# Kernel optimization log

Hardware: AMD Instinct MI355X
Metric: run time of the kernel (lower is better)

The kernel has to match this reference:

```python
import jax, jax.numpy as jnp
import numpy as np

N_NODES = 10000
N_EDGES = 320000
H = 256
L = 3
EPS = 1e-5


def _mlp2(x, w1, b1, w2, b2):
    # Linear -> ReLU -> Linear
    return jax.nn.relu(x @ w1 + b1) @ w2 + b2


def _layer_norm(x, g, b):
    mu = jnp.mean(x, axis=-1, keepdims=True)
    var = jnp.var(x, axis=-1, keepdims=True)
    return (x - mu) * jax.lax.rsqrt(var + EPS) * g + b


def setup_inputs() -> dict:
    key = jax.random.key(0)
    ks = jax.random.split(key, 24)
    s = 0.02
    inp = {
        "node_features": jax.random.normal(ks[0], (N_NODES, H), dtype=jnp.float32),
        "edge_index": jax.random.randint(ks[1], (2, N_EDGES), 0, N_NODES, dtype=jnp.int64),
        # node encoder (Linear 256->256, ReLU, Linear 256->256)
        "ne_w1": jax.random.normal(ks[2], (H, H), dtype=jnp.float32) * s,
        "ne_b1": jnp.zeros((H,), jnp.float32),
        "ne_w2": jax.random.normal(ks[3], (H, H), dtype=jnp.float32) * s,
        "ne_b2": jnp.zeros((H,), jnp.float32),
        # per-layer message MLP (2H->H, ReLU, H->H), stacked over L layers
        "msg_w1": jax.random.normal(ks[4], (L, 2 * H, H), dtype=jnp.float32) * s,
        "msg_b1": jnp.zeros((L, H), jnp.float32),
        "msg_w2": jax.random.normal(ks[5], (L, H, H), dtype=jnp.float32) * s,
        "msg_b2": jnp.zeros((L, H), jnp.float32),
        # per-layer update MLP (2H->H, ReLU, H->H)
        "upd_w1": jax.random.normal(ks[6], (L, 2 * H, H), dtype=jnp.float32) * s,
        "upd_b1": jnp.zeros((L, H), jnp.float32),
        "upd_w2": jax.random.normal(ks[7], (L, H, H), dtype=jnp.float32) * s,
        "upd_b2": jnp.zeros((L, H), jnp.float32),
        # per-layer LayerNorm
        "ln_g": jnp.ones((L, H), jnp.float32),
        "ln_b": jnp.zeros((L, H), jnp.float32),
        # readout MLP
        "ro_w1": jax.random.normal(ks[8], (H, H), dtype=jnp.float32) * s,
        "ro_b1": jnp.zeros((H,), jnp.float32),
        "ro_w2": jax.random.normal(ks[9], (H, H), dtype=jnp.float32) * s,
        "ro_b2": jnp.zeros((H,), jnp.float32),
    }
    return inp


def reference(node_features, edge_index, ne_w1, ne_b1, ne_w2, ne_b2,
              msg_w1, msg_b1, msg_w2, msg_b2,
              upd_w1, upd_b1, upd_w2, upd_b2,
              ln_g, ln_b, ro_w1, ro_b1, ro_w2, ro_b2):
    n_nodes = node_features.shape[0]
    src, dst = edge_index[0], edge_index[1]

    # node encoder
    x = _mlp2(node_features, ne_w1, ne_b1, ne_w2, ne_b2)  # [N, H]

    # message passing layers (edge_attr is unused in the original layer)
    for l in range(L):
        cat_e = jnp.concatenate([x[src], x[dst]], axis=-1)          # [E, 2H]
        messages = _mlp2(cat_e, msg_w1[l], msg_b1[l], msg_w2[l], msg_b2[l])  # [E, H]
        aggregated = jax.ops.segment_sum(messages, dst, num_segments=n_nodes)  # [N, H]
        cat_n = jnp.concatenate([x, aggregated], axis=-1)           # [N, 2H]
        updated = _mlp2(cat_n, upd_w1[l], upd_b1[l], upd_w2[l], upd_b2[l])
        x = _layer_norm(x + updated, ln_g[l], ln_b[l])

    # mean readout
    g = jnp.mean(x, axis=0)  # [H]
    return _mlp2(g, ro_w1, ro_b1, ro_w2, ro_b2)  # [H]
```

## Files before the change

kernel.cpp:

```cpp
#include <hip/hip_runtime.h>

#define NN 10000
#define NE 320000
#define HD 256
#define NL 3

typedef unsigned short ushort_t;
typedef __attribute__((ext_vector_type(8))) short bf16x8;
typedef __attribute__((ext_vector_type(4))) float f32x4;

#define MFMA __builtin_amdgcn_mfma_f32_16x16x32_bf16

__device__ __forceinline__ unsigned short f2bf(float x) {
    unsigned u = __float_as_uint(x);
    unsigned rounding = 0x7FFFu + ((u >> 16) & 1u);
    return (unsigned short)((u + rounding) >> 16);
}
__device__ __forceinline__ float bf2f(unsigned short u) {
    return __uint_as_float(((unsigned)u) << 16);
}
__device__ __forceinline__ bf16x8 cvt8(float4 lo, float4 hi) {
    bf16x8 r;
    r[0] = (short)f2bf(lo.x); r[1] = (short)f2bf(lo.y);
    r[2] = (short)f2bf(lo.z); r[3] = (short)f2bf(lo.w);
    r[4] = (short)f2bf(hi.x); r[5] = (short)f2bf(hi.y);
    r[6] = (short)f2bf(hi.z); r[7] = (short)f2bf(hi.w);
    return r;
}
__device__ __forceinline__ void dma16(const void* g, void* l) {
    __builtin_amdgcn_global_load_lds(
        (const __attribute__((address_space(1))) unsigned int*)g,
        (__attribute__((address_space(3))) unsigned int*)l, 16, 0, 0);
}


__global__ void hist_deg(const int* __restrict__ dst, int* __restrict__ deg, int E) {
    int e = blockIdx.x * blockDim.x + threadIdx.x;
    if (e < E) atomicAdd(&deg[dst[e]], 1);
}

__global__ __launch_bounds__(1024) void scan_csr(const int* __restrict__ deg,
                                                 int* __restrict__ row_start,
                                                 int* __restrict__ cursor,
                                                 float* __restrict__ degf,
                                                 float* __restrict__ gsum, int n) {
    __shared__ int wsum[16];
    __shared__ int carry_s;
    int tid = threadIdx.x, lane = tid & 63, wid = tid >> 6;
    if (tid < HD) gsum[tid] = 0.f;
    if (tid == 0) carry_s = 0;
    __syncthreads();
    for (int base = 0; base < n; base += 1024) {
        int i = base + tid;
        int v = (i < n) ? deg[i] : 0;
        int s = v;
        #pragma unroll
        for (int off = 1; off < 64; off <<= 1) {
            int t = __shfl_up(s, off);
            if (lane >= off) s += t;
        }
        if (lane == 63) wsum[wid] = s;
        __syncthreads();
        if (wid == 0 && lane < 16) {
            int ws = wsum[lane];
            #pragma unroll
            for (int off = 1; off < 16; off <<= 1) {
                int t = __shfl_up(ws, off);
                if (lane >= off) ws += t;
            }
            wsum[lane] = ws;
        }
        __syncthreads();
        int carry = carry_s;
        int wpre = (wid > 0) ? wsum[wid - 1] : 0;
        int incl = carry + wpre + s;
        int excl = incl - v;
        if (i < n) { row_start[i] = excl; cursor[i] = excl; degf[i] = (float)v; }
        __syncthreads();
        if (tid == 1023) carry_s = incl;
        __syncthreads();
    }
    if (tid == 0) row_start[n] = carry_s;
}

__global__ void scatter_src(const int* __restrict__ src, const int* __restrict__ dst,
                            int* __restrict__ cursor, int* __restrict__ src_sorted, int E) {
    int e = blockIdx.x * blockDim.x + threadIdx.x;
    if (e < E) {
        int pos = atomicAdd(&cursor[dst[e]], 1);
        src_sorted[pos] = src[e];
    }
}


struct TDesc { const float* src; ushort_t* dst; int transpose; };
struct TArgs { TDesc d[20]; };

__global__ __launch_bounds__(256) void conv_t(TArgs args) {
    __shared__ ushort_t tile[64][65];
    const float* src = args.d[blockIdx.y].src;
    ushort_t* dst = args.d[blockIdx.y].dst;
    int tr = args.d[blockIdx.y].transpose;
    int t = blockIdx.x;
    int r0 = (t >> 2) * 64, c0 = (t & 3) * 64;
    int tid = threadIdx.x;
    int rr = tid >> 4, cc4 = (tid & 15) * 4;
    if (!tr) {
        #pragma unroll
        for (int i = 0; i < 4; ++i) {
            int r = r0 + rr + i * 16;
            float4 v = *(const float4*)(src + (size_t)r * HD + c0 + cc4);
            ushort4 o = { f2bf(v.x), f2bf(v.y), f2bf(v.z), f2bf(v.w) };
            *(ushort4*)(dst + (size_t)r * HD + c0 + cc4) = o;
        }
        return;
    }
    #pragma unroll
    for (int i = 0; i < 4; ++i) {
        int r = rr + i * 16;
        float4 v = *(const float4*)(src + (size_t)(r0 + r) * HD + c0 + cc4);
        tile[cc4 + 0][r] = f2bf(v.x);
        tile[cc4 + 1][r] = f2bf(v.y);
        tile[cc4 + 2][r] = f2bf(v.z);
        tile[cc4 + 3][r] = f2bf(v.w);
    }
    __syncthreads();
    #pragma unroll
    for (int i = 0; i < 4; ++i) {
        int c = rr + i * 16;
        ushort4 o = { tile[c][cc4], tile[c][cc4 + 1], tile[c][cc4 + 2], tile[c][cc4 + 3] };
        *(ushort4*)(dst + (size_t)(c0 + c) * HD + r0 + cc4) = o;
    }
}

__global__ __launch_bounds__(256) void bias_compose(const float* __restrict__ mb2,
                                                    const float* __restrict__ uw1,
                                                    float* __restrict__ out) {
    int l = blockIdx.x, c = threadIdx.x;
    const float* b2l = mb2 + (size_t)l * HD;
    const float* u1b = uw1 + (size_t)l * 2 * HD * HD + (size_t)HD * HD;
    float s = 0.f;
    for (int k = 0; k < HD; ++k) s += b2l[k] * u1b[(size_t)k * HD + c];
    out[(size_t)l * HD + c] = s;
}

__global__ __launch_bounds__(256) void gemm_w2u(
    const ushort_t* __restrict__ Abase, const ushort_t* __restrict__ Btbase,
    ushort_t* __restrict__ outBase)
{
    const ushort_t* A  = Abase  + (size_t)blockIdx.z * HD * HD;
    const ushort_t* Bt = Btbase + (size_t)blockIdx.z * HD * HD;
    ushort_t* outB     = outBase + (size_t)blockIdx.z * HD * HD;
    int tid = threadIdx.x;
    int wid = tid >> 6, lane = tid & 63;
    int wm = wid >> 1, wn = wid & 1;
    int row0 = blockIdx.x * 64 + wm * 32;
    int col0 = blockIdx.y * 64 + wn * 32;
    int lm = lane & 15, lk = (lane >> 4) * 8;
    f32x4 acc[2][2] = {};
    const ushort_t* a0p = A + (size_t)(row0 + lm) * HD + lk;
    const ushort_t* a1p = A + (size_t)(row0 + 16 + lm) * HD + lk;
    const ushort_t* b0p = Bt + (size_t)(col0 + lm) * HD + lk;
    const ushort_t* b1p = Bt + (size_t)(col0 + 16 + lm) * HD + lk;
    #pragma unroll
    for (int k0 = 0; k0 < HD; k0 += 32) {
        bf16x8 a0 = *(const bf16x8*)(a0p + k0);
        bf16x8 a1 = *(const bf16x8*)(a1p + k0);
        bf16x8 b0 = *(const bf16x8*)(b0p + k0);
        bf16x8 b1 = *(const bf16x8*)(b1p + k0);
        acc[0][0] = MFMA(a0, b0, acc[0][0], 0, 0, 0);
        acc[0][1] = MFMA(a0, b1, acc[0][1], 0, 0, 0);
        acc[1][0] = MFMA(a1, b0, acc[1][0], 0, 0, 0);
        acc[1][1] = MFMA(a1, b1, acc[1][1], 0, 0, 0);
    }
    int orow = (lane >> 4) * 4;
    #pragma unroll
    for (int mi = 0; mi < 2; ++mi)
        #pragma unroll
        for (int r = 0; r < 4; ++r) {
            int row = row0 + mi * 16 + orow + r;
            #pragma unroll
            for (int ni = 0; ni < 2; ++ni) {
                int col = col0 + ni * 16 + lm;
                outB[(size_t)row * HD + col] = f2bf(acc[mi][ni][r]);
            }
        }
}

__device__ __forceinline__ int swz(int row, int byte_in_row) {
    return row * 512 + (byte_in_row ^ ((row & 7) << 4));
}


__global__ __launch_bounds__(512, 4) void enc_pq(
    const float* __restrict__ A, const ushort_t* __restrict__ B1t,
    const ushort_t* __restrict__ B2t,
    const float* __restrict__ b1, const float* __restrict__ b2,
    const ushort_t* __restrict__ Pw1t, const ushort_t* __restrict__ Pw1b,
    const float* __restrict__ pqb1,
    float* __restrict__ xF, ushort_t* __restrict__ xB,
    ushort_t* __restrict__ P, float* __restrict__ Q, int M)
{
    __shared__ char wbuf[2][2][16384];
    __shared__ char hid[16 * 512];
    int tid = threadIdx.x;
    int w = tid >> 6, lane = tid & 63;
    int lm = lane & 15, q = lane >> 4;
    int row0 = blockIdx.x * 16;
    int col0 = w * 32;
    int cA = col0 + lm, cB = col0 + 16 + lm;

    auto stageB = [&](const ushort_t* Bt, int k0, char* dst16k, int cc) {
        int col = cc * 16 + (lane >> 2);
        int qs = (lane & 3) ^ (col & 3) ^ ((col >> 2) & 3);
        dma16((const char*)Bt + (size_t)col * 512 + k0 * 2 + qs * 16, dst16k + cc * 1024);
    };
    auto readB = [&](const char* base, int ni) -> bf16x8 {
        int col = col0 + 16 * ni + lm;
        int q2 = q ^ (col & 3) ^ ((col >> 2) & 3);
        return *(const bf16x8*)(base + col * 64 + q2 * 16);
    };

    for (int c = w; c < 16; c += 8) stageB(B1t, 0, wbuf[0][0], c);

    float b1v[2] = { b1[cA], b1[cB] };
    float b2v[2] = { b2[cA], b2[cB] };
    float pqv[2] = { pqb1[cA], pqb1[cB] };
    bf16x8 areg[8];
    {
        const float* ap = A + (size_t)(row0 + lm) * HD + q * 8;
        #pragma unroll
        for (int j = 0; j < 8; ++j) {
            float4 lo = *(const float4*)(ap + j * 32);
            float4 hi = *(const float4*)(ap + j * 32 + 4);
            areg[j] = cvt8(lo, hi);
        }
    }
    __syncthreads();

    f32x4 acc[2] = {};
    #pragma unroll
    for (int j = 0; j < 8; ++j) {
        if (j < 7) {
            int k0 = (j + 1) * 32, p = (j + 1) & 1;
            for (int c = w; c < 16; c += 8) stageB(B1t, k0, wbuf[p][0], c);
        }
        int p = j & 1;
        acc[0] = MFMA(areg[j], readB(wbuf[p][0], 0), acc[0], 0, 0, 0);
        acc[1] = MFMA(areg[j], readB(wbuf[p][0], 1), acc[1], 0, 0, 0);
        __syncthreads();
    }

    for (int c = w; c < 16; c += 8) stageB(B2t, 0, wbuf[0][0], c);
    #pragma unroll
    for (int ni = 0; ni < 2; ++ni) {
        int col = col0 + 16 * ni + lm;
        #pragma unroll
        for (int r = 0; r < 4; ++r) {
            int row = 4 * q + r;
            float v = fmaxf(acc[ni][r] + b1v[ni], 0.f);
            *(ushort_t*)(hid + swz(row, col * 2)) = f2bf(v);
        }
    }
    __syncthreads();

    f32x4 acc2[2] = {};
    #pragma unroll
    for (int j = 0; j < 8; ++j) {
        if (j < 7) {
            int k0 = (j + 1) * 32, p = (j + 1) & 1;
            for (int c = w; c < 16; c += 8) stageB(B2t, k0, wbuf[p][0], c);
        }
        int p = j & 1;
        int bk = (j * 32 + q * 8) * 2;
        bf16x8 a = *(const bf16x8*)(hid + swz(lm, bk));
        acc2[0] = MFMA(a, readB(wbuf[p][0], 0), acc2[0], 0, 0, 0);
        acc2[1] = MFMA(a, readB(wbuf[p][0], 1), acc2[1], 0, 0, 0);
        __syncthreads();
    }

    for (int c = w; c < 32; c += 8) {
        if (c < 16) stageB(Pw1t, 0, wbuf[0][0], c);
        else        stageB(Pw1b, 0, wbuf[0][1], c - 16);
    }
    #pragma unroll
    for (int ni = 0; ni < 2; ++ni) {
        int col = col0 + 16 * ni + lm;
        #pragma unroll
        for (int r = 0; r < 4; ++r) {
            int row = 4 * q + r;
            int grow = row0 + row;
            float v = acc2[ni][r] + b2v[ni];
            *(ushort_t*)(hid + swz(row, col * 2)) = f2bf(v);
            xF[(size_t)grow * HD + col] = v;
            xB[(size_t)grow * HD + col] = f2bf(v);
        }
    }
    __syncthreads();

    f32x4 aP[2] = {}, aQ[2] = {};
    #pragma unroll
    for (int j = 0; j < 8; ++j) {
        if (j < 7) {
            int k0 = (j + 1) * 32, p = (j + 1) & 1;
            for (int c = w; c < 32; c += 8) {
                if (c < 16) stageB(Pw1t, k0, wbuf[p][0], c);
                else        stageB(Pw1b, k0, wbuf[p][1], c - 16);
            }
        }
        int p = j & 1;
        int bk = (j * 32 + q * 8) * 2;
        bf16x8 a = *(const bf16x8*)(hid + swz(lm, bk));
        #pragma unroll
        for (int ni = 0; ni < 2; ++ni) {
            aP[ni] = MFMA(a, readB(wbuf[p][0], ni), aP[ni], 0, 0, 0);
            aQ[ni] = MFMA(a, readB(wbuf[p][1], ni), aQ[ni], 0, 0, 0);
        }
        __syncthreads();
    }
    #pragma unroll
    for (int r = 0; r < 4; ++r) {
        int grow = row0 + 4 * q + r;
        #pragma unroll
        for (int ni = 0; ni < 2; ++ni) {
            int col = col0 + 16 * ni + lm;
            P[(size_t)grow * HD + col] = f2bf(aP[ni][r]);
            Q[(size_t)grow * HD + col] = aQ[ni][r] + pqv[ni];
        }
    }
}


__global__ __launch_bounds__(256) void edge_agg(
    const ushort_t* __restrict__ Pb, const float* __restrict__ Qf,
    const int* __restrict__ row_start, const int* __restrict__ srcs,
    ushort_t* __restrict__ Haggb)
{
    int node = blockIdx.x * 4 + (threadIdx.x >> 6);
    int lane = threadIdx.x & 63;
    int c4 = lane * 4;
    float4 qb = *(const float4*)(Qf + (size_t)node * HD + c4);
    float4 acc = {0.f, 0.f, 0.f, 0.f};
    int j = row_start[node], e = row_start[node + 1];
    for (; j + 8 <= e; j += 8) {
        ushort4 p[8];
        #pragma unroll
        for (int u = 0; u < 8; ++u) {
            int s = srcs[j + u];
            p[u] = *(const ushort4*)(Pb + (size_t)s * HD + c4);
        }
        #pragma unroll
        for (int u = 0; u < 8; ++u) {
            acc.x += fmaxf(bf2f(p[u].x) + qb.x, 0.f);
            acc.y += fmaxf(bf2f(p[u].y) + qb.y, 0.f);
            acc.z += fmaxf(bf2f(p[u].z) + qb.z, 0.f);
            acc.w += fmaxf(bf2f(p[u].w) + qb.w, 0.f);
        }
    }
    for (; j < e; ++j) {
        int s0 = srcs[j];
        ushort4 p0 = *(const ushort4*)(Pb + (size_t)s0 * HD + c4);
        acc.x += fmaxf(bf2f(p0.x) + qb.x, 0.f);
        acc.y += fmaxf(bf2f(p0.y) + qb.y, 0.f);
        acc.z += fmaxf(bf2f(p0.z) + qb.z, 0.f);
        acc.w += fmaxf(bf2f(p0.w) + qb.w, 0.f);
    }
    ushort4 o = { f2bf(acc.x), f2bf(acc.y), f2bf(acc.z), f2bf(acc.w) };
    *(ushort4*)(Haggb + (size_t)node * HD + c4) = o;
}


__global__ __launch_bounds__(512, 4) void upd_ln(
    const ushort_t* __restrict__ xb, const ushort_t* __restrict__ Hb,
    const ushort_t* __restrict__ B1t, const ushort_t* __restrict__ B2t,
    const ushort_t* __restrict__ B3t,
    const float* __restrict__ degf,
    const float* __restrict__ b1, const float* __restrict__ bias2,
    const float* __restrict__ b3,
    const float* __restrict__ g, const float* __restrict__ bb,
    const ushort_t* __restrict__ Pw1t, const ushort_t* __restrict__ Pw1b,
    const float* __restrict__ pqb1,
    float* __restrict__ gsum,
    float* __restrict__ xF, ushort_t* __restrict__ xB,
    ushort_t* __restrict__ P, float* __restrict__ Q, int M)
{
    __shared__ char wbuf[2][2][16384];
    __shared__ char abuf[2][2][1024];
    __shared__ char hid[16 * 512];
    __shared__ float sS[8][16], sQ[8][16], muv[16], ivv[16];

    int tid = threadIdx.x;
    int w = tid >> 6, lane = tid & 63;
    int lm = lane & 15, q = lane >> 4;
    int row0 = blockIdx.x * 16;
    int col0 = w * 32;
    int cA = col0 + lm, cB = col0 + 16 + lm;

    float b1v[2] = { b1[cA], b1[cB] };
    float bzv[2] = { bias2[cA], bias2[cB] };
    float b3v[2] = { b3[cA], b3[cB] };
    float gv[2]  = { g[cA],  g[cB]  };
    float bbv[2] = { bb[cA], bb[cB] };
    float pqv[2] = { Pw1t ? pqb1[cA] : 0.f, Pw1t ? pqb1[cB] : 0.f };
    float dgv[4], res[2][4];
    #pragma unroll
    for (int r = 0; r < 4; ++r) {
        int row = 4 * q + r;
        dgv[r] = degf[row0 + row];
        res[0][r] = xF[(size_t)(row0 + row) * HD + cA];
        res[1][r] = xF[(size_t)(row0 + row) * HD + cB];
    }

    auto stageB = [&](const ushort_t* Bt, int k0, char* dst16k, int cc) {
        int col = cc * 16 + (lane >> 2);
        int qs = (lane & 3) ^ (col & 3) ^ ((col >> 2) & 3);
        dma16((const char*)Bt + (size_t)col * 512 + k0 * 2 + qs * 16, dst16k + cc * 1024);
    };
    auto stageA = [&](const ushort_t* X, int k0, char* dst1k) {
        int row = lane >> 2;
        int qs = (lane & 3) ^ (row & 3) ^ ((row >> 2) & 3);
        dma16((const char*)X + (size_t)(row0 + row) * 512 + k0 * 2 + qs * 16, dst1k);
    };
    auto readB = [&](const char* base, int ni) -> bf16x8 {
        int col = col0 + 16 * ni + lm;
        int q2 = q ^ (col & 3) ^ ((col >> 2) & 3);
        return *(const bf16x8*)(base + col * 64 + q2 * 16);
    };
    auto readA = [&](const char* base) -> bf16x8 {
        int q2 = q ^ (lm & 3) ^ ((lm >> 2) & 3);
        return *(const bf16x8*)(base + lm * 64 + q2 * 16);
    };

    auto stage1 = [&](int j, int p) {
        int k0 = j * 32;
        for (int c = w; c < 34; c += 8) {
            if (c < 16)       stageB(B1t, k0, wbuf[p][0], c);
            else if (c < 32)  stageB(B2t, k0, wbuf[p][1], c - 16);
            else if (c == 32) stageA(xb, k0, abuf[p][0]);
            else              stageA(Hb, k0, abuf[p][1]);
        }
    };
    f32x4 acc[2] = {};
    stage1(0, 0);
    __syncthreads();
    #pragma unroll
    for (int j = 0; j < 8; ++j) {
        if (j < 7) stage1(j + 1, (j + 1) & 1);
        int p = j & 1;
        bf16x8 ax = readA(abuf[p][0]);
        bf16x8 ah = readA(abuf[p][1]);
        #pragma unroll
        for (int ni = 0; ni < 2; ++ni) {
            bf16x8 bu = readB(wbuf[p][0], ni);
            bf16x8 bw = readB(wbuf[p][1], ni);
            acc[ni] = MFMA(ax, bu, acc[ni], 0, 0, 0);
            acc[ni] = MFMA(ah, bw, acc[ni], 0, 0, 0);
        }
        __syncthreads();
    }

    for (int c = w; c < 16; c += 8) stageB(B3t, 0, wbuf[0][0], c);
    #pragma unroll
    for (int r = 0; r < 4; ++r) {
        int row = 4 * q + r;
        #pragma unroll
        for (int ni = 0; ni < 2; ++ni) {
            int col = col0 + 16 * ni + lm;
            float v = fmaxf(acc[ni][r] + b1v[ni] + dgv[r] * bzv[ni], 0.f);
            *(ushort_t*)(hid + swz(row, col * 2)) = f2bf(v);
        }
    }
    __syncthreads();

    f32x4 acc2[2] = {};
    #pragma unroll
    for (int j = 0; j < 8; ++j) {
        if (j < 7) {
            int k0 = (j + 1) * 32, p = (j + 1) & 1;
            for (int c = w; c < 16; c += 8) stageB(B3t, k0, wbuf[p][0], c);
        }
        int p = j & 1;
        int bk = (j * 32 + q * 8) * 2;
        bf16x8 a = *(const bf16x8*)(hid + swz(lm, bk));
        #pragma unroll
        for (int ni = 0; ni < 2; ++ni) {
            bf16x8 b = readB(wbuf[p][0], ni);
            acc2[ni] = MFMA(a, b, acc2[ni], 0, 0, 0);
        }
        __syncthreads();
    }

    if (Pw1t) {
        for (int c = w; c < 32; c += 8) {
            if (c < 16) stageB(Pw1t, 0, wbuf[0][0], c);
            else        stageB(Pw1b, 0, wbuf[0][1], c - 16);
        }
    }
    #pragma unroll
    for (int r = 0; r < 4; ++r) {
        float s = 0.f, qq = 0.f;
        #pragma unroll
        for (int ni = 0; ni < 2; ++ni) {
            float v = acc2[ni][r] + b3v[ni] + res[ni][r];
            acc2[ni][r] = v;
            s += v; qq += v * v;
        }
        #pragma unroll
        for (int off = 1; off < 16; off <<= 1) {
            s += __shfl_xor(s, off);
            qq += __shfl_xor(qq, off);
        }
        if (lm == 0) {
            int row = 4 * q + r;
            sS[w][row] = s; sQ[w][row] = qq;
        }
    }
    __syncthreads();
    if (tid < 16) {
        float s = 0.f, qq = 0.f;
        #pragma unroll
        for (int i = 0; i < 8; ++i) { s += sS[i][tid]; qq += sQ[i][tid]; }
        float mu = s * (1.0f / HD);
        float var = qq * (1.0f / HD) - mu * mu;
        muv[tid] = mu;
        ivv[tid] = rsqrtf(var + 1e-5f);
    }
    __syncthreads();
    float csum[2] = {0.f, 0.f};
    #pragma unroll
    for (int r = 0; r < 4; ++r) {
        int row = 4 * q + r;
        int grow = row0 + row;
        float mu = muv[row], iv = ivv[row];
        #pragma unroll
        for (int ni = 0; ni < 2; ++ni) {
            int col = col0 + 16 * ni + lm;
            float o = (acc2[ni][r] - mu) * iv * gv[ni] + bbv[ni];
            *(ushort_t*)(hid + swz(row, col * 2)) = f2bf(o);
            xF[(size_t)grow * HD + col] = o;
            xB[(size_t)grow * HD + col] = f2bf(o);
            csum[ni] += o;
        }
    }
    if (gsum) {
        #pragma unroll
        for (int ni = 0; ni < 2; ++ni) {
            float s = csum[ni];
            s += __shfl_xor(s, 16);
            s += __shfl_xor(s, 32);
            if (q == 0) atomicAdd(&gsum[col0 + 16 * ni + lm], s);
        }
    }

    if (Pw1t) {
        __syncthreads();
        f32x4 aP[2] = {}, aQ[2] = {};
        #pragma unroll
        for (int j = 0; j < 8; ++j) {
            if (j < 7) {
                int k0 = (j + 1) * 32, p = (j + 1) & 1;
                for (int c = w; c < 32; c += 8) {
                    if (c < 16) stageB(Pw1t, k0, wbuf[p][0], c);
                    else        stageB(Pw1b, k0, wbuf[p][1], c - 16);
                }
            }
            int p = j & 1;
            int bk = (j * 32 + q * 8) * 2;
            bf16x8 a = *(const bf16x8*)(hid + swz(lm, bk));
            #pragma unroll
            for (int ni = 0; ni < 2; ++ni) {
                bf16x8 bp = readB(wbuf[p][0], ni);
                bf16x8 bq = readB(wbuf[p][1], ni);
                aP[ni] = MFMA(a, bp, aP[ni], 0, 0, 0);
                aQ[ni] = MFMA(a, bq, aQ[ni], 0, 0, 0);
            }
            __syncthreads();
        }
        #pragma unroll
        for (int r = 0; r < 4; ++r) {
            int grow = row0 + 4 * q + r;
            #pragma unroll
            for (int ni = 0; ni < 2; ++ni) {
                int col = col0 + 16 * ni + lm;
                P[(size_t)grow * HD + col] = f2bf(aP[ni][r]);
                Q[(size_t)grow * HD + col] = aQ[ni][r] + pqv[ni];
            }
        }
    }
}


__global__ __launch_bounds__(256) void readout_mlp(
    const float* __restrict__ gsum,
    const float* __restrict__ w1, const float* __restrict__ b1,
    const float* __restrict__ w2, const float* __restrict__ b2,
    float* __restrict__ out, float invn)
{
    __shared__ float gl[HD], h1[HD];
    int c = threadIdx.x;
    gl[c] = gsum[c] * invn;
    __syncthreads();
    float a = b1[c];
    for (int k = 0; k < HD; ++k) a += gl[k] * w1[k * HD + c];
    h1[c] = fmaxf(a, 0.f);
    __syncthreads();
    float o = b2[c];
    for (int k = 0; k < HD; ++k) o += h1[k] * w2[k * HD + c];
    out[c] = o;
}


extern "C" void kernel_launch(void* const* d_in, const int* in_sizes, int n_in,
                              void* d_out, int out_size, void* d_ws, size_t ws_size,
                              hipStream_t stream) {
    const float* nf    = (const float*)d_in[0];
    const int*   ei    = (const int*)d_in[1];
    const float* ne_w1 = (const float*)d_in[2];
    const float* ne_b1 = (const float*)d_in[3];
    const float* ne_w2 = (const float*)d_in[4];
    const float* ne_b2 = (const float*)d_in[5];
    const float* mw1   = (const float*)d_in[6];
    const float* mb1   = (const float*)d_in[7];
    const float* mw2   = (const float*)d_in[8];
    const float* mb2   = (const float*)d_in[9];
    const float* uw1   = (const float*)d_in[10];
    const float* ub1   = (const float*)d_in[11];
    const float* uw2   = (const float*)d_in[12];
    const float* ub2   = (const float*)d_in[13];
    const float* lng   = (const float*)d_in[14];
    const float* lnb   = (const float*)d_in[15];
    const float* rw1   = (const float*)d_in[16];
    const float* rb1   = (const float*)d_in[17];
    const float* rw2   = (const float*)d_in[18];
    const float* rb2   = (const float*)d_in[19];

    const int* e_src = ei;
    const int* e_dst = ei + NE;

    char* w = (char*)d_ws;
    size_t off = 0;
    auto alloc = [&](size_t bytes) -> void* {
        void* p = w + off;
        off = (off + bytes + 255) & ~(size_t)255;
        return p;
    };
    const size_t NF32 = (size_t)NN * HD * sizeof(float);
    const size_t NF16 = (size_t)NN * HD * sizeof(ushort_t);
    const size_t WM16 = (size_t)HD * HD * sizeof(ushort_t);

    float* x    = (float*)alloc(NF32);
    float* Qf   = (float*)alloc(NF32);
    float* gsum = (float*)alloc(HD * sizeof(float));
    float* degf = (float*)alloc(NN * sizeof(float));
    float* b2u1 = (float*)alloc(NL * HD * sizeof(float));

    ushort_t* xb    = (ushort_t*)alloc(NF16);
    ushort_t* Pb    = (ushort_t*)alloc(NF16);
    ushort_t* Haggb = (ushort_t*)alloc(NF16);
    ushort_t* neT1  = (ushort_t*)alloc(WM16);
    ushort_t* neT2  = (ushort_t*)alloc(WM16);
    ushort_t* w1tT  = (ushort_t*)alloc(NL * WM16);
    ushort_t* w1bT  = (ushort_t*)alloc(NL * WM16);
    ushort_t* u1tT  = (ushort_t*)alloc(NL * WM16);
    ushort_t* u1bT  = (ushort_t*)alloc(NL * WM16);
    ushort_t* u2T   = (ushort_t*)alloc(NL * WM16);
    ushort_t* w2uT  = (ushort_t*)alloc(NL * WM16);
    ushort_t* w2rmb = (ushort_t*)alloc(NL * WM16);

    int* deg       = (int*)alloc(NN * sizeof(int));
    int* row_start = (int*)alloc((NN + 1) * sizeof(int));
    int* cursor    = (int*)alloc(NN * sizeof(int));
    int* srcs      = (int*)alloc(NE * sizeof(int));

    hipMemsetAsync(deg, 0, NN * sizeof(int), stream);

    hist_deg<<<(NE + 255) / 256, 256, 0, stream>>>(e_dst, deg, NE);
    scan_csr<<<1, 1024, 0, stream>>>(deg, row_start, cursor, degf, gsum, NN);
    scatter_src<<<(NE + 255) / 256, 256, 0, stream>>>(e_src, e_dst, cursor, srcs, NE);

    TArgs ta;
    ta.d[0] = { ne_w1, neT1, 1 };
    ta.d[1] = { ne_w2, neT2, 1 };
    for (int l = 0; l < NL; ++l) {
        const float* w1l = mw1 + (size_t)l * 2 * HD * HD;
        const float* u1l = uw1 + (size_t)l * 2 * HD * HD;
        ta.d[2 + l]  = { w1l,                       w1tT + (size_t)l * HD * HD, 1 };
        ta.d[5 + l]  = { w1l + (size_t)HD * HD,     w1bT + (size_t)l * HD * HD, 1 };
        ta.d[8 + l]  = { u1l,                       u1tT + (size_t)l * HD * HD, 1 };
        ta.d[11 + l] = { u1l + (size_t)HD * HD,     u1bT + (size_t)l * HD * HD, 1 };
        ta.d[14 + l] = { uw2 + (size_t)l * HD * HD, u2T + (size_t)l * HD * HD, 1 };
        ta.d[17 + l] = { mw2 + (size_t)l * HD * HD, w2rmb + (size_t)l * HD * HD, 0 };
    }
    conv_t<<<dim3(16, 20), 256, 0, stream>>>(ta);
    bias_compose<<<NL, 256, 0, stream>>>(mb2, uw1, b2u1);
    gemm_w2u<<<dim3(4, 4, NL), 256, 0, stream>>>(u1bT, w2rmb, w2uT);

    enc_pq<<<NN / 16, 512, 0, stream>>>(nf, neT1, neT2, ne_b1, ne_b2,
                                        w1tT, w1bT, mb1, x, xb, Pb, Qf, NN);

    for (int l = 0; l < NL; ++l) {
        edge_agg<<<NN / 4, 256, 0, stream>>>(Pb, Qf, row_start, srcs, Haggb);
        int nl = l + 1;
        const ushort_t* pw1t = (nl < NL) ? w1tT + (size_t)nl * HD * HD : nullptr;
        const ushort_t* pw1b = (nl < NL) ? w1bT + (size_t)nl * HD * HD : nullptr;
        const float*    pqb1 = (nl < NL) ? mb1 + (size_t)nl * HD : nullptr;
        float* gs = (l == NL - 1) ? gsum : nullptr;
        upd_ln<<<NN / 16, 512, 0, stream>>>(
            xb, Haggb, u1tT + (size_t)l * HD * HD, w2uT + (size_t)l * HD * HD,
            u2T + (size_t)l * HD * HD, degf,
            ub1 + (size_t)l * HD, b2u1 + (size_t)l * HD, ub2 + (size_t)l * HD,
            lng + (size_t)l * HD, lnb + (size_t)l * HD,
            pw1t, pw1b, pqb1, gs, x, xb, Pb, Qf, NN);
    }

    readout_mlp<<<1, 256, 0, stream>>>(gsum, rw1, rb1, rw2, rb2, (float*)d_out, 1.0f / NN);
}
```

Measured before the change: 326.6 us.

## Pipeline weight DMA two stages ahead with explicit vmcnt waits in node kernels

```diff
diff --git a/kernel.cpp b/kernel.cpp
--- a/kernel.cpp
+++ b/kernel.cpp
@@ -10,6 +10,11 @@
 typedef __attribute__((ext_vector_type(4))) float f32x4;
 
 #define MFMA __builtin_amdgcn_mfma_f32_16x16x32_bf16
+
+#define WAITV(N) asm volatile("s_waitcnt vmcnt(" #N ")" ::: "memory")
+#define HARDBAR() do { __builtin_amdgcn_s_barrier(); __builtin_amdgcn_sched_barrier(0); } while (0)
+#define LGKMBAR() do { asm volatile("s_waitcnt lgkmcnt(0)" ::: "memory"); \
+                       __builtin_amdgcn_s_barrier(); __builtin_amdgcn_sched_barrier(0); } while (0)
 
 __device__ __forceinline__ unsigned short f2bf(float x) {
     unsigned u = __float_as_uint(x);
@@ -210,10 +215,25 @@
     int col0 = w * 32;
     int cA = col0 + lm, cB = col0 + 16 + lm;
 
-    auto stageB = [&](const ushort_t* Bt, int k0, char* dst16k, int cc) {
-        int col = cc * 16 + (lane >> 2);
-        int qs = (lane & 3) ^ (col & 3) ^ ((col >> 2) & 3);
-        dma16((const char*)Bt + (size_t)col * 512 + k0 * 2 + qs * 16, dst16k + cc * 1024);
+    auto stage1 = [&](const ushort_t* M0, int k0, int p) {
+        #pragma unroll
+        for (int i = 0; i < 2; ++i) {
+            int cc = 2 * w + i;
+            int col = cc * 16 + (lane >> 2);
+            int qs = (lane & 3) ^ (col & 3) ^ ((col >> 2) & 3);
+            dma16((const char*)M0 + (size_t)col * 512 + k0 * 2 + qs * 16, wbuf[p][0] + cc * 1024);
+        }
+    };
+    auto stage2 = [&](const ushort_t* M0, const ushort_t* M1, int k0, int p) {
+        #pragma unroll
+        for (int i = 0; i < 4; ++i) {
+            int c = 4 * w + i;
+            int m = c >> 4, cc = c & 15;
+            const ushort_t* Mt = m ? M1 : M0;
+            int col = cc * 16 + (lane >> 2);
+            int qs = (lane & 3) ^ (col & 3) ^ ((col >> 2) & 3);
+            dma16((const char*)Mt + (size_t)col * 512 + k0 * 2 + qs * 16, wbuf[p][m] + cc * 1024);
+        }
     };
     auto readB = [&](const char* base, int ni) -> bf16x8 {
         int col = col0 + 16 * ni + lm;
@@ -221,8 +241,8 @@
         return *(const bf16x8*)(base + col * 64 + q2 * 16);
     };
 
-    for (int c = w; c < 16; c += 8) stageB(B1t, 0, wbuf[0][0], c);
-
+    stage1(B1t, 0, 0);
+    stage1(B1t, 32, 1);
     float b1v[2] = { b1[cA], b1[cB] };
     float b2v[2] = { b2[cA], b2[cB] };
     float pqv[2] = { pqb1[cA], pqb1[cB] };
@@ -236,22 +256,21 @@
             areg[j] = cvt8(lo, hi);
         }
     }
-    __syncthreads();
 
     f32x4 acc[2] = {};
     #pragma unroll
     for (int j = 0; j < 8; ++j) {
-        if (j < 7) {
-            int k0 = (j + 1) * 32, p = (j + 1) & 1;
-            for (int c = w; c < 16; c += 8) stageB(B1t, k0, wbuf[p][0], c);
-        }
         int p = j & 1;
+        if (j < 7) { WAITV(2); } else { WAITV(0); }
+        HARDBAR();
         acc[0] = MFMA(areg[j], readB(wbuf[p][0], 0), acc[0], 0, 0, 0);
         acc[1] = MFMA(areg[j], readB(wbuf[p][0], 1), acc[1], 0, 0, 0);
-        __syncthreads();
-    }
-
-    for (int c = w; c < 16; c += 8) stageB(B2t, 0, wbuf[0][0], c);
+        LGKMBAR();
+        if (j < 6) stage1(B1t, (j + 2) * 32, p);
+    }
+
+    stage1(B2t, 0, 0);
+    stage1(B2t, 32, 1);
     #pragma unroll
     for (int ni = 0; ni < 2; ++ni) {
         int col = col0 + 16 * ni + lm;
@@ -262,27 +281,24 @@
             *(ushort_t*)(hid + swz(row, col * 2)) = f2bf(v);
         }
     }
-    __syncthreads();
+    LGKMBAR();
 
     f32x4 acc2[2] = {};
     #pragma unroll
     for (int j = 0; j < 8; ++j) {
-        if (j < 7) {
-            int k0 = (j + 1) * 32, p = (j + 1) & 1;
-            for (int c = w; c < 16; c += 8) stageB(B2t, k0, wbuf[p][0], c);
-        }
         int p = j & 1;
+        if (j < 7) { WAITV(2); } else { WAITV(0); }
+        HARDBAR();
         int bk = (j * 32 + q * 8) * 2;
         bf16x8 a = *(const bf16x8*)(hid + swz(lm, bk));
         acc2[0] = MFMA(a, readB(wbuf[p][0], 0), acc2[0], 0, 0, 0);
         acc2[1] = MFMA(a, readB(wbuf[p][0], 1), acc2[1], 0, 0, 0);
-        __syncthreads();
-    }
-
-    for (int c = w; c < 32; c += 8) {
-        if (c < 16) stageB(Pw1t, 0, wbuf[0][0], c);
-        else        stageB(Pw1b, 0, wbuf[0][1], c - 16);
-    }
+        LGKMBAR();
+        if (j < 6) stage1(B2t, (j + 2) * 32, p);
+    }
+
+    stage2(Pw1t, Pw1b, 0, 0);
+    stage2(Pw1t, Pw1b, 32, 1);
     #pragma unroll
     for (int ni = 0; ni < 2; ++ni) {
         int col = col0 + 16 * ni + lm;
@@ -296,19 +312,14 @@
             xB[(size_t)grow * HD + col] = f2bf(v);
         }
     }
-    __syncthreads();
+    LGKMBAR();
 
     f32x4 aP[2] = {}, aQ[2] = {};
     #pragma unroll
     for (int j = 0; j < 8; ++j) {
-        if (j < 7) {
-            int k0 = (j + 1) * 32, p = (j + 1) & 1;
-            for (int c = w; c < 32; c += 8) {
-                if (c < 16) stageB(Pw1t, k0, wbuf[p][0], c);
-                else        stageB(Pw1b, k0, wbuf[p][1], c - 16);
-            }
-        }
         int p = j & 1;
+        if (j < 7) { WAITV(4); } else { WAITV(0); }
+        HARDBAR();
         int bk = (j * 32 + q * 8) * 2;
         bf16x8 a = *(const bf16x8*)(hid + swz(lm, bk));
         #pragma unroll
@@ -316,7 +327,8 @@
             aP[ni] = MFMA(a, readB(wbuf[p][0], ni), aP[ni], 0, 0, 0);
             aQ[ni] = MFMA(a, readB(wbuf[p][1], ni), aQ[ni], 0, 0, 0);
         }
-        __syncthreads();
+        LGKMBAR();
+        if (j < 6) stage2(Pw1t, Pw1b, (j + 2) * 32, p);
     }
     #pragma unroll
     for (int r = 0; r < 4; ++r) {
@@ -385,7 +397,6 @@
     ushort_t* __restrict__ P, float* __restrict__ Q, int M)
 {
     __shared__ char wbuf[2][2][16384];
-    __shared__ char abuf[2][2][1024];
     __shared__ char hid[16 * 512];
     __shared__ float sS[8][16], sQ[8][16], muv[16], ivv[16];
 
@@ -396,6 +407,45 @@
     int col0 = w * 32;
     int cA = col0 + lm, cB = col0 + 16 + lm;
 
+    auto stage1 = [&](const ushort_t* M0, int k0, int p) {
+        #pragma unroll
+        for (int i = 0; i < 2; ++i) {
+            int cc = 2 * w + i;
+            int col = cc * 16 + (lane >> 2);
+            int qs = (lane & 3) ^ (col & 3) ^ ((col >> 2) & 3);
+            dma16((const char*)M0 + (size_t)col * 512 + k0 * 2 + qs * 16, wbuf[p][0] + cc * 1024);
+        }
+    };
+    auto stage2 = [&](const ushort_t* M0, const ushort_t* M1, int k0, int p) {
+        #pragma unroll
+        for (int i = 0; i < 4; ++i) {
+            int c = 4 * w + i;
+            int m = c >> 4, cc = c & 15;
+            const ushort_t* Mt = m ? M1 : M0;
+            int col = cc * 16 + (lane >> 2);
+            int qs = (lane & 3) ^ (col & 3) ^ ((col >> 2) & 3);
+            dma16((const char*)Mt + (size_t)col * 512 + k0 * 2 + qs * 16, wbuf[p][m] + cc * 1024);
+        }
+    };
+    auto readB = [&](const char* base, int ni) -> bf16x8 {
+        int col = col0 + 16 * ni + lm;
+        int q2 = q ^ (col & 3) ^ ((col >> 2) & 3);
+        return *(const bf16x8*)(base + col * 64 + q2 * 16);
+    };
+
+    stage2(B1t, B2t, 0, 0);
+    stage2(B1t, B2t, 32, 1);
+
+    bf16x8 axr[8], ahr[8];
+    {
+        const ushort_t* xp = xb + (size_t)(row0 + lm) * HD + q * 8;
+        const ushort_t* hp = Hb + (size_t)(row0 + lm) * HD + q * 8;
+        #pragma unroll
+        for (int j = 0; j < 8; ++j) {
+            axr[j] = *(const bf16x8*)(xp + j * 32);
+            ahr[j] = *(const bf16x8*)(hp + j * 32);
+        }
+    }
     float b1v[2] = { b1[cA], b1[cB] };
     float bzv[2] = { bias2[cA], bias2[cB] };
     float b3v[2] = { b3[cA], b3[cB] };
@@ -411,55 +461,23 @@
         res[1][r] = xF[(size_t)(row0 + row) * HD + cB];
     }
 
-    auto stageB = [&](const ushort_t* Bt, int k0, char* dst16k, int cc) {
-        int col = cc * 16 + (lane >> 2);
-        int qs = (lane & 3) ^ (col & 3) ^ ((col >> 2) & 3);
-        dma16((const char*)Bt + (size_t)col * 512 + k0 * 2 + qs * 16, dst16k + cc * 1024);
-    };
-    auto stageA = [&](const ushort_t* X, int k0, char* dst1k) {
-        int row = lane >> 2;
-        int qs = (lane & 3) ^ (row & 3) ^ ((row >> 2) & 3);
-        dma16((const char*)X + (size_t)(row0 + row) * 512 + k0 * 2 + qs * 16, dst1k);
-    };
-    auto readB = [&](const char* base, int ni) -> bf16x8 {
-        int col = col0 + 16 * ni + lm;
-        int q2 = q ^ (col & 3) ^ ((col >> 2) & 3);
-        return *(const bf16x8*)(base + col * 64 + q2 * 16);
-    };
-    auto readA = [&](const char* base) -> bf16x8 {
-        int q2 = q ^ (lm & 3) ^ ((lm >> 2) & 3);
-        return *(const bf16x8*)(base + lm * 64 + q2 * 16);
-    };
-
-    auto stage1 = [&](int j, int p) {
-        int k0 = j * 32;
-        for (int c = w; c < 34; c += 8) {
-            if (c < 16)       stageB(B1t, k0, wbuf[p][0], c);
-            else if (c < 32)  stageB(B2t, k0, wbuf[p][1], c - 16);
-            else if (c == 32) stageA(xb, k0, abuf[p][0]);
-            else              stageA(Hb, k0, abuf[p][1]);
-        }
-    };
     f32x4 acc[2] = {};
-    stage1(0, 0);
-    __syncthreads();
     #pragma unroll
     for (int j = 0; j < 8; ++j) {
-        if (j < 7) stage1(j + 1, (j + 1) & 1);
         int p = j & 1;
-        bf16x8 ax = readA(abuf[p][0]);
-        bf16x8 ah = readA(abuf[p][1]);
+        if (j < 7) { WAITV(4); } else { WAITV(0); }
+        HARDBAR();
         #pragma unroll
         for (int ni = 0; ni < 2; ++ni) {
-            bf16x8 bu = readB(wbuf[p][0], ni);
-            bf16x8 bw = readB(wbuf[p][1], ni);
-            acc[ni] = MFMA(ax, bu, acc[ni], 0, 0, 0);
-            acc[ni] = MFMA(ah, bw, acc[ni], 0, 0, 0);
-        }
-        __syncthreads();
-    }
-
-    for (int c = w; c < 16; c += 8) stageB(B3t, 0, wbuf[0][0], c);
+            acc[ni] = MFMA(axr[j], readB(wbuf[p][0], ni), acc[ni], 0, 0, 0);
+            acc[ni] = MFMA(ahr[j], readB(wbuf[p][1], ni), acc[ni], 0, 0, 0);
+        }
+        LGKMBAR();
+        if (j < 6) stage2(B1t, B2t, (j + 2) * 32, p);
+    }
+
+    stage1(B3t, 0, 0);
+    stage1(B3t, 32, 1);
     #pragma unroll
     for (int r = 0; r < 4; ++r) {
         int row = 4 * q + r;
@@ -470,31 +488,25 @@
             *(ushort_t*)(hid + swz(row, col * 2)) = f2bf(v);
         }
     }
-    __syncthreads();
+    LGKMBAR();
 
     f32x4 acc2[2] = {};
     #pragma unroll
     for (int j = 0; j < 8; ++j) {
-        if (j < 7) {
-            int k0 = (j + 1) * 32, p = (j + 1) & 1;
-            for (int c = w; c < 16; c += 8) stageB(B3t, k0, wbuf[p][0], c);
-        }
         int p = j & 1;
+        if (j < 7) { WAITV(2); } else { WAITV(0); }
+        HARDBAR();
         int bk = (j * 32 + q * 8) * 2;
         bf16x8 a = *(const bf16x8*)(hid + swz(lm, bk));
-        #pragma unroll
-        for (int ni = 0; ni < 2; ++ni) {
-            bf16x8 b = readB(wbuf[p][0], ni);
-            acc2[ni] = MFMA(a, b, acc2[ni], 0, 0, 0);
-        }
-        __syncthreads();
+        acc2[0] = MFMA(a, readB(wbuf[p][0], 0), acc2[0], 0, 0, 0);
+        acc2[1] = MFMA(a, readB(wbuf[p][0], 1), acc2[1], 0, 0, 0);
+        LGKMBAR();
+        if (j < 6) stage1(B3t, (j + 2) * 32, p);
     }
 
     if (Pw1t) {
-        for (int c = w; c < 32; c += 8) {
-            if (c < 16) stageB(Pw1t, 0, wbuf[0][0], c);
-            else        stageB(Pw1b, 0, wbuf[0][1], c - 16);
-        }
+        stage2(Pw1t, Pw1b, 0, 0);
+        stage2(Pw1t, Pw1b, 32, 1);
     }
     #pragma unroll
     for (int r = 0; r < 4; ++r) {
@@ -515,7 +527,7 @@
             sS[w][row] = s; sQ[w][row] = qq;
         }
     }
-    __syncthreads();
+    LGKMBAR();
     if (tid < 16) {
         float s = 0.f, qq = 0.f;
         #pragma unroll
@@ -525,7 +537,7 @@
         muv[tid] = mu;
         ivv[tid] = rsqrtf(var + 1e-5f);
     }
-    __syncthreads();
+    LGKMBAR();
     float csum[2] = {0.f, 0.f};
     #pragma unroll
     for (int r = 0; r < 4; ++r) {
@@ -553,28 +565,22 @@
     }
 
     if (Pw1t) {
-        __syncthreads();
+        LGKMBAR();
         f32x4 aP[2] = {}, aQ[2] = {};
         #pragma unroll
         for (int j = 0; j < 8; ++j) {
-            if (j < 7) {
-                int k0 = (j + 1) * 32, p = (j + 1) & 1;
-                for (int c = w; c < 32; c += 8) {
-                    if (c < 16) stageB(Pw1t, k0, wbuf[p][0], c);
-                    else        stageB(Pw1b, k0, wbuf[p][1], c - 16);
-                }
-            }
             int p = j & 1;
+            if (j < 7) { WAITV(4); } else { WAITV(0); }
+            HARDBAR();
             int bk = (j * 32 + q * 8) * 2;
             bf16x8 a = *(const bf16x8*)(hid + swz(lm, bk));
             #pragma unroll
             for (int ni = 0; ni < 2; ++ni) {
-                bf16x8 bp = readB(wbuf[p][0], ni);
-                bf16x8 bq = readB(wbuf[p][1], ni);
-                aP[ni] = MFMA(a, bp, aP[ni], 0, 0, 0);
-                aQ[ni] = MFMA(a, bq, aQ[ni], 0, 0, 0);
+                aP[ni] = MFMA(a, readB(wbuf[p][0], ni), aP[ni], 0, 0, 0);
+                aQ[ni] = MFMA(a, readB(wbuf[p][1], ni), aQ[ni], 0, 0, 0);
             }
-            __syncthreads();
+            LGKMBAR();
+            if (j < 6) stage2(Pw1t, Pw1b, (j + 2) * 32, p);
         }
         #pragma unroll
         for (int r = 0; r < 4; ++r) {
```

After: 369.3 us. 13.1% more time.
